# Optimization experiments

Hardware: AMD Instinct MI355X
Metric: run time of the kernel (lower is better)

The kernel has to match this reference:

```python
import jax, jax.numpy as jnp
import numpy as np


def setup_inputs() -> dict:
    key = jax.random.key(0)
    x = jax.random.normal(key, (128, 256, 32, 32), dtype=jnp.float32)
    return {"x": x, "topk": 5}


def reference(x, topk):
    B = x.shape[0]
    flat = x.reshape(B, -1)                      # [B, N]
    _, idx = jax.lax.top_k(flat, topk)           # [B, k] indices into N
    out = jnp.zeros_like(flat)
    out = out.at[jnp.arange(B)[:, None], idx].set(1.0)
    return out.reshape(x.shape)
```

## Files before the change

kernel.cpp:

```cpp
#include <hip/hip_runtime.h>
#include <limits.h>
#include <math.h>
#include <stdint.h>

#define BROWS 128
#define NCOLS (256 * 32 * 32)
#define K 5
#define BPR 32
#define TPB 256
#define CHUNK (NCOLS / BPR)
#define F4T (CHUNK / 4 / TPB)
#define WPR (BPR * 4)
#define NFLAG 16
#define CAP 256

typedef float v4f __attribute__((ext_vector_type(4)));

__device__ __forceinline__ uint64_t make_key(float f, uint32_t idx) {
    uint32_t u = __float_as_uint(f);
    u = (u & 0x80000000u) ? ~u : (u | 0x80000000u);
    return ((uint64_t)u << 32) | (uint32_t)(~idx);
}
__device__ __forceinline__ uint32_t key_idx(uint64_t k) { return ~(uint32_t)k; }

#define KEY_NEG_INF 0x007FFFFF00000000ULL

__device__ __forceinline__ void insert5(uint64_t (&key)[K], uint64_t c) {
    if (c > key[K - 1]) {
        key[K - 1] = c;
#pragma unroll
        for (int s = K - 1; s > 0; --s) {
            if (key[s] > key[s - 1]) {
                uint64_t t = key[s]; key[s] = key[s - 1]; key[s - 1] = t;
            }
        }
    }
}

__device__ __forceinline__ void wave_reduce5(uint64_t (&key)[K]) {
#pragma unroll
    for (int off = 1; off < 64; off <<= 1) {
        uint64_t ok[K];
#pragma unroll
        for (int k = 0; k < K; ++k)
            ok[k] = __shfl_xor((unsigned long long)key[k], off, 64);
#pragma unroll
        for (int k = 0; k < K; ++k) insert5(key, ok[k]);
    }
}

__device__ __forceinline__ void insert5f(float (&v)[K], float c) {
    if (c > v[K - 1]) {
        v[K - 1] = c;
#pragma unroll
        for (int s = K - 1; s > 0; --s) {
            if (v[s] > v[s - 1]) { float t = v[s]; v[s] = v[s - 1]; v[s - 1] = t; }
        }
    }
}

__global__ __launch_bounds__(TPB) void wta_stream(const float* __restrict__ x,
                                                  float* __restrict__ out,
                                                  float* __restrict__ wmax) {
    const int gb = blockIdx.x;
    const size_t base = (size_t)gb * CHUNK;
    const float4* __restrict__ x4 = (const float4*)(x + base);
    v4f* __restrict__ o4 = (v4f*)(out + base);
    const int t = threadIdx.x;
    const v4f z = {0.f, 0.f, 0.f, 0.f};

    float4 d[F4T];
#pragma unroll
    for (int j = 0; j < F4T; ++j) d[j] = x4[t + j * TPB];
#pragma unroll
    for (int j = 0; j < F4T; ++j)
        __builtin_nontemporal_store(z, &o4[t + j * TPB]);

    float M = -INFINITY;
#pragma unroll
    for (int j = 0; j < F4T; ++j)
        M = fmaxf(M, fmaxf(fmaxf(d[j].x, d[j].y), fmaxf(d[j].z, d[j].w)));
#pragma unroll
    for (int off = 1; off < 64; off <<= 1)
        M = fmaxf(M, __shfl_xor(M, off, 64));

    if ((t & 63) == 0) wmax[gb * 4 + (t >> 6)] = M;
}

__global__ __launch_bounds__(TPB) void wta_finish(const float* __restrict__ x,
                                                  const float* __restrict__ wmax,
                                                  float* __restrict__ out) {
    const int row = blockIdx.x;
    const int t = threadIdx.x;
    const float* __restrict__ wm = wmax + row * WPR;

    __shared__ float sT;
    __shared__ int nflag, ncand;
    __shared__ int flaglist[NFLAG];
    __shared__ uint64_t cand[CAP];

    if (t == 0) { nflag = 0; ncand = 0; }
    __syncthreads();

    if (t < 64) {
        float v[K];
#pragma unroll
        for (int k = 0; k < K; ++k) v[k] = -INFINITY;
        insert5f(v, wm[t]);
        insert5f(v, wm[t + 64]);
#pragma unroll
        for (int off = 1; off < 64; off <<= 1) {
            float ov[K];
#pragma unroll
            for (int k = 0; k < K; ++k) ov[k] = __shfl_xor(v[k], off, 64);
#pragma unroll
            for (int k = 0; k < K; ++k) insert5f(v, ov[k]);
        }
        if (t == 0) sT = v[K - 1];
    }
    __syncthreads();
    const float T = sT;

    if (t < WPR && wm[t] >= T) {
        const int s = atomicAdd(&nflag, 1);
        if (s < NFLAG) flaglist[s] = t;
    }
    __syncthreads();
    const int nf = min(nflag, NFLAG);

    const int lane = t & 63, jj = t >> 6;
    for (int f = 0; f < nf; ++f) {
        const int wid = flaglist[f];
        const int gbk = wid >> 2;
        const int w   = wid & 3;
        const float4* __restrict__ xb =
            (const float4*)(x + (size_t)row * NCOLS + (size_t)gbk * CHUNK);
#pragma unroll
        for (int rep = 0; rep < 2; ++rep) {
            const int j = jj + rep * 4;
            const int f4pos = w * 64 + lane + j * TPB;
            const float4 d = xb[f4pos];
            const float vs[4] = {d.x, d.y, d.z, d.w};
#pragma unroll
            for (int c = 0; c < 4; ++c) {
                if (vs[c] >= T) {
                    const int s = atomicAdd(&ncand, 1);
                    if (s < CAP)
                        cand[s] = make_key(vs[c],
                                           (uint32_t)gbk * CHUNK + (uint32_t)f4pos * 4u + c);
                }
            }
        }
    }
    __syncthreads();

    if (t < 64) {
        const int n = min(ncand, CAP);
        uint64_t key[K];
#pragma unroll
        for (int k = 0; k < K; ++k) key[k] = KEY_NEG_INF;
        for (int i = t; i < n; i += 64) insert5(key, cand[i]);
        wave_reduce5(key);
        if (t == 0) {
#pragma unroll
            for (int k = 0; k < K; ++k)
                if (key[k] != KEY_NEG_INF)
                    out[(size_t)row * NCOLS + key_idx(key[k])] = 1.0f;
        }
    }
}

extern "C" void kernel_launch(void* const* d_in, const int* in_sizes, int n_in,
                              void* d_out, int out_size, void* d_ws, size_t ws_size,
                              hipStream_t stream) {
    const float* x = (const float*)d_in[0];
    float* out = (float*)d_out;

    float* wmax = (float*)d_ws;

    wta_stream<<<BROWS * BPR, TPB, 0, stream>>>(x, out, wmax);
    wta_finish<<<BROWS, TPB, 0, stream>>>(x, wmax, out);
}
```

Baseline: 244.3 us.

## Make stream kernel persistent with register double-buffered chunk prefetch

Measured after the change: 248.4 us. Within noise of the previous version (+1.7%).

```diff
diff --git a/kernel.cpp b/kernel.cpp
--- a/kernel.cpp
+++ b/kernel.cpp
@@ -9,8 +9,11 @@
 #define BPR 32
 #define TPB 256
 #define CHUNK (NCOLS / BPR)
-#define F4T (CHUNK / 4 / TPB)
+#define C4 (CHUNK / 4)
+#define F4T (C4 / TPB)
 #define WPR (BPR * 4)
+#define SBLK 512
+#define ITERS ((BROWS * BPR) / SBLK)
 #define NFLAG 16
 #define CAP 256
 
@@ -62,29 +65,54 @@
 __global__ __launch_bounds__(TPB) void wta_stream(const float* __restrict__ x,
                                                   float* __restrict__ out,
                                                   float* __restrict__ wmax) {
-    const int gb = blockIdx.x;
-    const size_t base = (size_t)gb * CHUNK;
-    const float4* __restrict__ x4 = (const float4*)(x + base);
-    v4f* __restrict__ o4 = (v4f*)(out + base);
+    const int b = blockIdx.x;
     const int t = threadIdx.x;
+    const int lane = t & 63, w = t >> 6;
+    const int c0 = b * ITERS;
+    const float4* __restrict__ x4 = (const float4*)x;
+    v4f* __restrict__ o4 = (v4f*)out;
     const v4f z = {0.f, 0.f, 0.f, 0.f};
-
-    float4 d[F4T];
-#pragma unroll
-    for (int j = 0; j < F4T; ++j) d[j] = x4[t + j * TPB];
-#pragma unroll
-    for (int j = 0; j < F4T; ++j)
-        __builtin_nontemporal_store(z, &o4[t + j * TPB]);
-
-    float M = -INFINITY;
-#pragma unroll
-    for (int j = 0; j < F4T; ++j)
-        M = fmaxf(M, fmaxf(fmaxf(d[j].x, d[j].y), fmaxf(d[j].z, d[j].w)));
-#pragma unroll
-    for (int off = 1; off < 64; off <<= 1)
-        M = fmaxf(M, __shfl_xor(M, off, 64));
-
-    if ((t & 63) == 0) wmax[gb * 4 + (t >> 6)] = M;
+    const size_t base0 = (size_t)c0 * C4;
+
+    float4 a[F4T];
+#pragma unroll
+    for (int j = 0; j < F4T; ++j) a[j] = x4[base0 + t + j * TPB];
+
+#pragma unroll 1
+    for (int it = 0; it < ITERS - 1; ++it) {
+        const size_t cb = base0 + (size_t)it * C4;
+        float4 nb[F4T];
+#pragma unroll
+        for (int j = 0; j < F4T; ++j) nb[j] = x4[cb + C4 + t + j * TPB];
+#pragma unroll
+        for (int j = 0; j < F4T; ++j)
+            __builtin_nontemporal_store(z, &o4[cb + t + j * TPB]);
+        float M = -INFINITY;
+#pragma unroll
+        for (int j = 0; j < F4T; ++j)
+            M = fmaxf(M, fmaxf(fmaxf(a[j].x, a[j].y), fmaxf(a[j].z, a[j].w)));
+#pragma unroll
+        for (int off = 1; off < 64; off <<= 1)
+            M = fmaxf(M, __shfl_xor(M, off, 64));
+        if (lane == 0) wmax[(c0 + it) * 4 + w] = M;
+#pragma unroll
+        for (int j = 0; j < F4T; ++j) a[j] = nb[j];
+    }
+
+    {
+        const size_t cb = base0 + (size_t)(ITERS - 1) * C4;
+#pragma unroll
+        for (int j = 0; j < F4T; ++j)
+            __builtin_nontemporal_store(z, &o4[cb + t + j * TPB]);
+        float M = -INFINITY;
+#pragma unroll
+        for (int j = 0; j < F4T; ++j)
+            M = fmaxf(M, fmaxf(fmaxf(a[j].x, a[j].y), fmaxf(a[j].z, a[j].w)));
+#pragma unroll
+        for (int off = 1; off < 64; off <<= 1)
+            M = fmaxf(M, __shfl_xor(M, off, 64));
+        if (lane == 0) wmax[(c0 + ITERS - 1) * 4 + w] = M;
+    }
 }
 
 __global__ __launch_bounds__(TPB) void wta_finish(const float* __restrict__ x,
@@ -178,6 +206,6 @@
 
     float* wmax = (float*)d_ws;
 
-    wta_stream<<<BROWS * BPR, TPB, 0, stream>>>(x, out, wmax);
+    wta_stream<<<SBLK, TPB, 0, stream>>>(x, out, wmax);
     wta_finish<<<BROWS, TPB, 0, stream>>>(x, wmax, out);
 }
```
